# Kernel optimization log

Measured on AMD Instinct MI355X. Metric: run time of the kernel, lower is better.

## Reference

```python
import jax, jax.numpy as jnp
import numpy as np

ALPHA = 0.2          # LeakyReLU negative slope
N = 4096             # num nodes
E = 262144           # num edges (avg degree 64)
NFEAT = 512
NHID = 64
NHEAD = 8
NCLASS = 16
NEG_INF = -1e20


def setup_inputs() -> dict:
    key = jax.random.key(0)
    ks = jax.random.split(key, 8)
    features = jax.random.normal(ks[0], (N, NFEAT), dtype=jnp.float32)
    edge_list = jax.random.randint(ks[1], (2, E), 0, N, dtype=jnp.int64)
    # xavier-uniform-ish init scaled like gain=1.414
    W_heads = jax.random.normal(ks[2], (NHEAD, NFEAT, NHID), dtype=jnp.float32) * (1.414 / np.sqrt(NFEAT))
    a_heads = jax.random.normal(ks[3], (NHEAD, 2 * NHID, 1), dtype=jnp.float32) * 0.1
    b_heads = jnp.zeros((NHEAD, NHID), dtype=jnp.float32)
    W_out = jax.random.normal(ks[4], (NHEAD * NHID, NCLASS), dtype=jnp.float32) * (1.414 / np.sqrt(NHEAD * NHID))
    a_out = jax.random.normal(ks[5], (2 * NCLASS, 1), dtype=jnp.float32) * 0.1
    b_out = jnp.zeros((NCLASS,), dtype=jnp.float32)
    return {
        "features": features, "edge_list": edge_list,
        "W_heads": W_heads, "a_heads": a_heads, "b_heads": b_heads,
        "W_out": W_out, "a_out": a_out, "b_out": b_out,
    }


def _gatconv(x, src, tgt, W, a, b):
    # dropout layers are identity in eval mode
    h = x @ W                                             # [N, F_out]
    # edge scores: gather endpoints, concat, project, LeakyReLU
    a_input = jnp.concatenate([h[src], h[tgt]], axis=1)   # [E, 2*F_out]
    e = jax.nn.leaky_relu((a_input @ a)[:, 0], ALPHA)     # [E]
    n = h.shape[0]
    # dense NxN attention: -1e20 default, edge scores scattered in
    att = jnp.full((n, n), NEG_INF, dtype=h.dtype).at[src, tgt].set(e)
    att = jax.nn.softmax(att, axis=1)                     # rows w/o edges -> uniform (matches torch)
    return att @ h + b                                    # [N, F_out]


def reference(features, edge_list, W_heads, a_heads, b_heads, W_out, a_out, b_out):
    src, tgt = edge_list[0], edge_list[1]
    # multi-head GATConv, heads vmapped over stacked params -> [H, N, NHID]
    heads = jax.vmap(lambda W, a, b: _gatconv(features, src, tgt, W, a, b))(
        W_heads, a_heads, b_heads)
    # torch.cat over heads on dim=1 == transpose+reshape
    x = jnp.transpose(heads, (1, 0, 2)).reshape(N, NHEAD * NHID)
    x = jax.nn.elu(x)
    out = _gatconv(x, src, tgt, W_out, a_out, b_out)      # [N, NCLASS]
    return jax.nn.log_softmax(out, axis=1)
```

## Files before the change

kernel.cpp:

```cpp
#include <hip/hip_runtime.h>
#include <hip/hip_bf16.h>

#define NN 4096
#define NFEAT 512
#define NHID 64
#define NHEAD 8
#define NCLASS 16
#define CAP 160
#define LALPHA 0.2f

#define SZ2 (NHEAD*2*NHID)
#define SZ3 (NHEAD*NHID)
#define SZ4 (NFEAT*NCLASS)
#define SZ5 (2*NCLASS)
#define SZ6 (NCLASS)
#define NSMALL (SZ2+SZ3+SZ4+SZ5+SZ6)
#define NGB 128

typedef __attribute__((ext_vector_type(8))) short bf16x8;
typedef __attribute__((ext_vector_type(4))) float f32x4;
typedef __attribute__((ext_vector_type(8))) unsigned short u16x8;

__device__ __forceinline__ float b2f(unsigned short h) {
    return __uint_as_float(((unsigned int)h) << 16);
}
__device__ __forceinline__ unsigned short f2b(float f) {
    unsigned int u = __float_as_uint(f);
    unsigned int r = (u + 0x7fffu + ((u >> 16) & 1u)) >> 16;
    return (unsigned short)r;
}
__device__ __forceinline__ float waveMax(float v) {
#pragma unroll
    for (int m = 32; m >= 1; m >>= 1) v = fmaxf(v, __shfl_xor(v, m, 64));
    return v;
}
__device__ __forceinline__ float waveSum(float v) {
#pragma unroll
    for (int m = 32; m >= 1; m >>= 1) v += __shfl_xor(v, m, 64);
    return v;
}
__device__ __forceinline__ float lrelu(float e) {
    return e >= 0.f ? e : LALPHA * e;
}

#if defined(__has_builtin)
#if __has_builtin(__builtin_amdgcn_fence)
#define GAT_HAS_FENCE 1
#endif
#endif
#ifdef GAT_HAS_FENCE
#define REL_FENCE() __builtin_amdgcn_fence(__ATOMIC_RELEASE, "agent")
#define ACQ_FENCE() __builtin_amdgcn_fence(__ATOMIC_ACQUIRE, "agent")
#else
#define REL_FENCE() __threadfence()
#define ACQ_FENCE() __threadfence()
#endif

__device__ __forceinline__ void gbar(int* gb, int idx, int nblk) {
    __syncthreads();
    if (threadIdx.x == 0) {
        REL_FENCE();
        int* ctr  = gb + idx * 32;
        int* flag = gb + idx * 32 + 16;
        int prev = __hip_atomic_fetch_add(ctr, 1, __ATOMIC_RELAXED,
                                          __HIP_MEMORY_SCOPE_AGENT);
        if (prev == nblk - 1) {
            __hip_atomic_store(flag, 1, __ATOMIC_RELAXED,
                               __HIP_MEMORY_SCOPE_AGENT);
        } else {
            while (__hip_atomic_load(flag, __ATOMIC_RELAXED,
                                     __HIP_MEMORY_SCOPE_AGENT) == 0)
                __builtin_amdgcn_s_sleep(8);
        }
        ACQ_FENCE();
    }
    __syncthreads();
}

__global__ void __launch_bounds__(256, 4)
k01(const void* __restrict__ f, const void* __restrict__ Wh_,
    const void* __restrict__ ah_, const void* __restrict__ bh_,
    const void* __restrict__ Wo_, const void* __restrict__ ao_,
    const void* __restrict__ bo_, const int* __restrict__ e32,
    int E, int csb,
    unsigned short* __restrict__ featb, unsigned short* __restrict__ Wtb,
    float* __restrict__ smallf, unsigned int* __restrict__ bits,
    unsigned short* __restrict__ Hb,
    float* __restrict__ s1, float* __restrict__ s2,
    float* __restrict__ cm1, int* __restrict__ gb) {
    __shared__ float tile[64][33];
    __shared__ float cms[64];
    __shared__ int sbf, s64f;
    int t = threadIdx.x, bid = blockIdx.x, nblk = gridDim.x;
    if (t < 64) {
        unsigned int w = ((const unsigned int*)f)[t];
        unsigned int lo = w & 0xffffu, e = (lo >> 7) & 0xffu;
        unsigned long long bal = __ballot(lo == 0u || (e >= 100u && e <= 140u));
        if (t == 0) sbf = (__popcll(bal) >= 40);
        unsigned long long bal2 = __ballot(e32[2 * t + 1] == 0);
        if (t == 0) s64f = (__popcll(bal2) >= 48);
    }
    __syncthreads();
    bool bf = (sbf != 0);
    for (int i = bid * 256 + t; i < NN * NN / 32; i += nblk * 256)
        bits[i] = 0u;
    for (int vb = bid; vb < 128; vb += nblk) {
        int h = vb >> 4, k0 = (vb & 15) * 32;
        int nn = t & 63, kh = t >> 6;
#pragma unroll
        for (int i = 0; i < 8; ++i) {
            int kk = kh * 8 + i;
            int si = (h << 15) + (k0 + kk) * NHID + nn;
            float v = bf ? b2f(((const unsigned short*)Wh_)[si])
                         : ((const float*)Wh_)[si];
            tile[nn][kk] = v;
        }
        __syncthreads();
        int n2 = t >> 2, kk0 = (t & 3) * 8;
        u16x8 o;
#pragma unroll
        for (int i = 0; i < 8; ++i) o[i] = f2b(tile[n2][kk0 + i]);
        *(u16x8*)&Wtb[(size_t)((h << 6) + n2) * NFEAT + k0 + kk0] = o;
        __syncthreads();
    }
    {
        const int NF8 = NN * NFEAT / 8;
        const int TOT = NF8 + NSMALL;
        int start = bf ? NF8 : 0;
        for (int i = start + bid * 256 + t; i < TOT; i += nblk * 256) {
            if (i < NF8) {
                float4 lo = ((const float4*)f)[i * 2];
                float4 hi = ((const float4*)f)[i * 2 + 1];
                u16x8 o;
                o[0] = f2b(lo.x); o[1] = f2b(lo.y); o[2] = f2b(lo.z); o[3] = f2b(lo.w);
                o[4] = f2b(hi.x); o[5] = f2b(hi.y); o[6] = f2b(hi.z); o[7] = f2b(hi.w);
                *(u16x8*)&featb[i * 8] = o;
            } else {
                int r = i - NF8;
                const void* sp; int off;
                if (r < SZ2)                        { sp = ah_; off = r; }
                else if (r < SZ2 + SZ3)             { sp = bh_; off = r - SZ2; }
                else if (r < SZ2 + SZ3 + SZ4)       { sp = Wo_; off = r - SZ2 - SZ3; }
                else if (r < SZ2 + SZ3 + SZ4 + SZ5) { sp = ao_; off = r - SZ2 - SZ3 - SZ4; }
                else                                { sp = bo_; off = r - SZ2 - SZ3 - SZ4 - SZ5; }
                smallf[r] = bf ? b2f(((const unsigned short*)sp)[off])
                               : ((const float*)sp)[off];
            }
        }
    }
    gbar(gb, 0, nblk);
    const unsigned short* Ab = bf ? (const unsigned short*)f : featb;
    const float* av8 = smallf;
    for (int tl = bid; tl < 256; tl += nblk) {
        if (t < 64) cms[t] = 0.f;
        __syncthreads();
        int w = t >> 6, l = t & 63;
        int quad = l >> 4, l16 = l & 15;
        int h = tl >> 5;
        int m0 = (tl & 31) * 128 + w * 32;
        f32x4 acc[2][4] = {};
        const unsigned short* a0p = Ab + (size_t)(m0 + l16) * NFEAT + quad * 8;
        const unsigned short* a1p = a0p + 16 * NFEAT;
        const unsigned short* bp  = Wtb + ((size_t)h << 15) + (size_t)l16 * NFEAT + quad * 8;
#pragma unroll 4
        for (int k0 = 0; k0 < NFEAT; k0 += 32) {
            bf16x8 a0 = *(const bf16x8*)(a0p + k0);
            bf16x8 a1 = *(const bf16x8*)(a1p + k0);
#pragma unroll
            for (int nt = 0; nt < 4; ++nt) {
                bf16x8 b = *(const bf16x8*)(bp + (size_t)nt * 16 * NFEAT + k0);
                acc[0][nt] = __builtin_amdgcn_mfma_f32_16x16x32_bf16(a0, b, acc[0][nt], 0, 0, 0);
                acc[1][nt] = __builtin_amdgcn_mfma_f32_16x16x32_bf16(a1, b, acc[1][nt], 0, 0, 0);
            }
        }
        const float* av = av8 + h * 2 * NHID;
        float p1[2][4] = {}, p2[2][4] = {};
#pragma unroll
        for (int rh = 0; rh < 2; ++rh) {
#pragma unroll
            for (int nt = 0; nt < 4; ++nt) {
                int col = nt * 16 + l16;
                float av1 = av[col], av2 = av[NHID + col];
                float csum = 0.f;
#pragma unroll
                for (int r = 0; r < 4; ++r) {
                    float v = acc[rh][nt][r];
                    int row = m0 + rh * 16 + quad * 4 + r;
                    Hb[((size_t)row << 9) + (h << 6) + col] = f2b(v);
                    p1[rh][r] += v * av1;
                    p2[rh][r] += v * av2;
                    csum += v;
                }
                atomicAdd(&cms[col], csum);
            }
        }
#pragma unroll
        for (int m = 8; m >= 1; m >>= 1)
#pragma unroll
            for (int rh = 0; rh < 2; ++rh)
#pragma unroll
                for (int r = 0; r < 4; ++r) {
                    p1[rh][r] += __shfl_xor(p1[rh][r], m, 64);
                    p2[rh][r] += __shfl_xor(p2[rh][r], m, 64);
                }
        if (l16 == 0) {
#pragma unroll
            for (int rh = 0; rh < 2; ++rh)
#pragma unroll
                for (int r = 0; r < 4; ++r) {
                    int row = m0 + rh * 16 + quad * 4 + r;
                    s1[(h << 12) + row] = p1[rh][r];
                    s2[(h << 12) + row] = p2[rh][r];
                }
        }
        __syncthreads();
        if (t < 64) atomicAdd(&cm1[h * NHID + t], cms[t]);
        __syncthreads();
    }
    for (int vb = bid; vb < csb; vb += nblk) {
        int i = vb * 256 + t;
        if (i < E) {
            int s, tt;
            if (s64f) { s = e32[2 * i]; tt = e32[2 * (E + i)]; }
            else      { s = e32[i];     tt = e32[E + i]; }
            s &= (NN - 1); tt &= (NN - 1);
            unsigned int pos = (unsigned int)s * NN + (unsigned int)tt;
            atomicOr(&bits[pos >> 5], 1u << (pos & 31u));
        }
    }
}

__global__ void __launch_bounds__(256, 4)
k23(const unsigned int* __restrict__ bits,
    const float* __restrict__ s1, const float* __restrict__ s2,
    const unsigned short* __restrict__ Hb,
    const float* __restrict__ bh, const float* __restrict__ cm1,
    const float* __restrict__ Wo, const float* __restrict__ ao,
    const float* __restrict__ bo,
    float* __restrict__ out2, float* __restrict__ s1o,
    float* __restrict__ s2o, float* __restrict__ cm2,
    float* __restrict__ outp, int* __restrict__ gb) {
    __shared__ float sW[4][CAP * 8];
    __shared__ int   sT[4][CAP];
    __shared__ float cms[NCLASS];
    __shared__ float o2s[4][16];
    int t = threadIdx.x, bid = blockIdx.x, nblk = gridDim.x;
    if (t < NCLASS) cms[t] = 0.f;
    int wid = t >> 6, lane = t & 63;
    int n = bid * 4 + wid;
    int d;
    {
        uint2 w2 = *(const uint2*)&bits[n * 128 + lane * 2];
        int c = __popc(w2.x) + __popc(w2.y);
        int incl = c;
#pragma unroll
        for (int off = 1; off < 64; off <<= 1) {
            int u = __shfl_up(incl, off, 64);
            if (lane >= off) incl += u;
        }
        int excl = incl - c;
        int total = __shfl(incl, 63, 64);
        int tbase = lane * 64;
        unsigned int x = w2.x;
        while (x) {
            int b = __ffs(x) - 1; x &= x - 1;
            if (excl < CAP) sT[wid][excl] = tbase + b;
            ++excl;
        }
        unsigned int y = w2.y;
        while (y) {
            int b = __ffs(y) - 1; y &= y - 1;
            if (excl < CAP) sT[wid][excl] = tbase + 32 + b;
            ++excl;
        }
        d = min(total, CAP);
    }
    __syncthreads();
    int h = lane >> 3, jslot = lane & 7;
    float acc[8] = {};
    float rden = 1.f;
    if (d > 0) {
        const float* s2h = s2 + ((size_t)h << 12);
        float s1n = s1[(h << 12) + n];
        float mx = -1e30f;
        for (int jb = 0; jb < d; jb += 8) {
            int j = jb + jslot;
            int tt = (j < d) ? sT[wid][j] : 0;
            float e = (j < d) ? lrelu(s1n + s2h[tt]) : -1e30f;
            sW[wid][(j << 3) + h] = e;
            mx = fmaxf(mx, e);
        }
        mx = fmaxf(mx, __shfl_xor(mx, 1, 64));
        mx = fmaxf(mx, __shfl_xor(mx, 2, 64));
        mx = fmaxf(mx, __shfl_xor(mx, 4, 64));
        float den = 0.f;
        for (int jb = 0; jb < d; jb += 8) {
            int j = jb + jslot;
            float e = sW[wid][(j << 3) + h];
            float w = __expf(e - mx);
            sW[wid][(j << 3) + h] = w;
            den += w;
        }
        den += __shfl_xor(den, 1, 64);
        den += __shfl_xor(den, 2, 64);
        den += __shfl_xor(den, 4, 64);
        rden = 1.f / den;
        const unsigned short* Hp = Hb + lane * 8;
        int j = 0;
        for (; j + 8 <= d; j += 8) {
            int tt[8]; float ww[8];
#pragma unroll
            for (int q = 0; q < 8; ++q) {
                tt[q] = sT[wid][j + q];
                ww[q] = sW[wid][((j + q) << 3) + h];
            }
            u16x8 vv[8];
#pragma unroll
            for (int q = 0; q < 8; ++q)
                vv[q] = *(const u16x8*)(Hp + ((size_t)tt[q] << 9));
#pragma unroll
            for (int q = 0; q < 8; ++q)
#pragma unroll
                for (int i = 0; i < 8; ++i)
                    acc[i] += ww[q] * b2f(vv[q][i]);
        }
        for (; j < d; ++j) {
            int t0 = sT[wid][j];
            float w0 = sW[wid][(j << 3) + h];
            u16x8 v0 = *(const u16x8*)(Hp + ((size_t)t0 << 9));
#pragma unroll
            for (int i = 0; i < 8; ++i) acc[i] += w0 * b2f(v0[i]);
        }
    }
    float o[8];
    if (d == 0) {
#pragma unroll
        for (int i = 0; i < 8; ++i) o[i] = cm1[lane * 8 + i] * (1.0f / NN);
    } else {
#pragma unroll
        for (int i = 0; i < 8; ++i) o[i] = acc[i] * rden;
    }
#pragma unroll
    for (int i = 0; i < 8; ++i) {
        float v = o[i] + bh[lane * 8 + i];
        o[i] = v > 0.f ? v : __expf(v) - 1.f;
    }
    float* xw = sW[wid];
    *(float4*)&xw[lane * 8]     = make_float4(o[0], o[1], o[2], o[3]);
    *(float4*)&xw[lane * 8 + 4] = make_float4(o[4], o[5], o[6], o[7]);
    int c = lane & 15, sub = lane >> 4;
    const float* xp = xw + sub * 128;
    const float* wp = Wo + sub * 128 * NCLASS + c;
    float a2 = 0.f;
#pragma unroll 8
    for (int kk = 0; kk < 128; ++kk) a2 += xp[kk] * wp[kk * NCLASS];
    a2 += __shfl_xor(a2, 16, 64);
    a2 += __shfl_xor(a2, 32, 64);
    if (lane < 16) out2[n * NCLASS + c] = a2;
    float r1 = a2 * ao[c], r2 = a2 * ao[NCLASS + c];
#pragma unroll
    for (int m = 8; m >= 1; m >>= 1) {
        r1 += __shfl_xor(r1, m, 16);
        r2 += __shfl_xor(r2, m, 16);
    }
    if (lane == 0) { s1o[n] = r1; s2o[n] = r2; }
    if (lane < 16) atomicAdd(&cms[c], a2);
    __syncthreads();
    if (t < NCLASS) atomicAdd(&cm2[t], cms[t]);

    gbar(gb, 1, nblk);

    {
        float val;
        if (d == 0) {
            val = cm2[c] * (1.0f / NN);
        } else {
            float s1n = s1o[n];
            float* wvw = sW[wid];
            int t0 = (lane < d)       ? sT[wid][lane]       : 0;
            int t1 = (lane + 64 < d)  ? sT[wid][lane + 64]  : 0;
            int t2 = (lane + 128 < d) ? sT[wid][lane + 128] : 0;
            float e0 = (lane < d)       ? lrelu(s1n + s2o[t0]) : -1e30f;
            float e1 = (lane + 64 < d)  ? lrelu(s1n + s2o[t1]) : -1e30f;
            float e2 = (lane + 128 < d) ? lrelu(s1n + s2o[t2]) : -1e30f;
            float m = waveMax(fmaxf(e0, fmaxf(e1, e2)));
            float w0 = (lane < d)       ? __expf(e0 - m) : 0.f;
            float w1 = (lane + 64 < d)  ? __expf(e1 - m) : 0.f;
            float w2 = (lane + 128 < d) ? __expf(e2 - m) : 0.f;
            float den = waveSum(w0 + w1 + w2);
            wvw[lane] = w0;
            wvw[lane + 64] = w1;
            if (lane + 128 < CAP) wvw[lane + 128] = w2;
            int g2 = lane >> 2, q = lane & 3;
            float a4[4] = {};
            for (int j = g2; j < d; j += 16) {
                float w = wvw[j];
                int tt = sT[wid][j];
                float4 v = *(const float4*)(out2 + tt * NCLASS + q * 4);
                a4[0] += w * v.x; a4[1] += w * v.y;
                a4[2] += w * v.z; a4[3] += w * v.w;
            }
#pragma unroll
            for (int m2 = 4; m2 <= 32; m2 <<= 1)
#pragma unroll
                for (int i = 0; i < 4; ++i) a4[i] += __shfl_xor(a4[i], m2, 64);
            if (lane < 4)
                *(float4*)&o2s[wid][lane * 4] = make_float4(a4[0], a4[1], a4[2], a4[3]);
            val = o2s[wid][c] / den;
        }
        val += bo[c];
        float mx = val;
#pragma unroll
        for (int m = 8; m >= 1; m >>= 1) mx = fmaxf(mx, __shfl_xor(mx, m, 16));
        float se = __expf(val - mx);
#pragma unroll
        for (int m = 8; m >= 1; m >>= 1) se += __shfl_xor(se, m, 16);
        float res = val - mx - __logf(se);
        if (lane < 16) outp[n * NCLASS + lane] = res;
    }
}

__global__ void __launch_bounds__(256)
k_prep0(const void* __restrict__ f, const void* __restrict__ Wh_,
        const void* __restrict__ ah_, const void* __restrict__ bh_,
        const void* __restrict__ Wo_, const void* __restrict__ ao_,
        const void* __restrict__ bo_,
        unsigned short* __restrict__ featb,
        unsigned short* __restrict__ Wtb,
        float* __restrict__ smallf,
        unsigned int* __restrict__ bits,
        float* __restrict__ cmz) {
    int t = threadIdx.x, bid = blockIdx.x;
    for (int i = bid * 256 + t; i < NN * NN / 32; i += gridDim.x * 256)
        bits[i] = 0u;
    if (bid == 0)
        for (int i = t; i < NHEAD * NHID + NCLASS; i += 256) cmz[i] = 0.f;
    __shared__ int sbf;
    if (t < 64) {
        unsigned int w = ((const unsigned int*)f)[t];
        unsigned int lo = w & 0xffffu, e = (lo >> 7) & 0xffu;
        unsigned long long bal = __ballot(lo == 0u || (e >= 100u && e <= 140u));
        if (t == 0) sbf = (__popcll(bal) >= 40);
    }
    __syncthreads();
    bool bf = (sbf != 0);
    if (bid < 128) {
        __shared__ float tile[64][33];
        int h = bid >> 4, k0 = (bid & 15) * 32;
        int n = t & 63, kh = t >> 6;
#pragma unroll
        for (int i = 0; i < 8; ++i) {
            int kk = kh * 8 + i;
            int si = (h << 15) + (k0 + kk) * NHID + n;
            float v = bf ? b2f(((const unsigned short*)Wh_)[si])
                         : ((const float*)Wh_)[si];
            tile[n][kk] = v;
        }
        __syncthreads();
        int n2 = t >> 2, kk0 = (t & 3) * 8;
        u16x8 o;
#pragma unroll
        for (int i = 0; i < 8; ++i) o[i] = f2b(tile[n2][kk0 + i]);
        *(u16x8*)&Wtb[(size_t)((h << 6) + n2) * NFEAT + k0 + kk0] = o;
    } else {
        const int NF8 = NN * NFEAT / 8;
        const int TOT = NF8 + NSMALL;
        int stride = (gridDim.x - 128) * 256;
        int start = bf ? NF8 : 0;
        for (int i = start + (bid - 128) * 256 + t; i < TOT; i += stride) {
            if (i < NF8) {
                float4 lo = ((const float4*)f)[i * 2];
                float4 hi = ((const float4*)f)[i * 2 + 1];
                u16x8 o;
                o[0] = f2b(lo.x); o[1] = f2b(lo.y); o[2] = f2b(lo.z); o[3] = f2b(lo.w);
                o[4] = f2b(hi.x); o[5] = f2b(hi.y); o[6] = f2b(hi.z); o[7] = f2b(hi.w);
                *(u16x8*)&featb[i * 8] = o;
            } else {
                int r = i - NF8;
                const void* sp; int off;
                if (r < SZ2)                        { sp = ah_; off = r; }
                else if (r < SZ2 + SZ3)             { sp = bh_; off = r - SZ2; }
                else if (r < SZ2 + SZ3 + SZ4)       { sp = Wo_; off = r - SZ2 - SZ3; }
                else if (r < SZ2 + SZ3 + SZ4 + SZ5) { sp = ao_; off = r - SZ2 - SZ3 - SZ4; }
                else                                { sp = bo_; off = r - SZ2 - SZ3 - SZ4 - SZ5; }
                smallf[r] = bf ? b2f(((const unsigned short*)sp)[off])
                               : ((const float*)sp)[off];
            }
        }
    }
}

__global__ void __launch_bounds__(256)
k_gemm_or(const void* __restrict__ f,
          const unsigned short* __restrict__ featb,
          const unsigned short* __restrict__ Wtb,
          const float* __restrict__ ah,
          unsigned short* __restrict__ Hb,
          float* __restrict__ s1, float* __restrict__ s2,
          float* __restrict__ cm1,
          const int* __restrict__ e32, int E,
          unsigned int* __restrict__ bits) {
    int t = threadIdx.x;
    if (blockIdx.x >= 256) {
        __shared__ int s64f;
        if (t < 64) {
            unsigned long long bal = __ballot(e32[2 * t + 1] == 0);
            if (t == 0) s64f = (__popcll(bal) >= 48);
        }
        __syncthreads();
        int i = (blockIdx.x - 256) * 256 + t;
        if (i < E) {
            int s, tt;
            if (s64f) { s = e32[2 * i]; tt = e32[2 * (E + i)]; }
            else      { s = e32[i];     tt = e32[E + i]; }
            s &= (NN - 1); tt &= (NN - 1);
            unsigned int pos = (unsigned int)s * NN + (unsigned int)tt;
            atomicOr(&bits[pos >> 5], 1u << (pos & 31u));
        }
        return;
    }
    __shared__ int sbf;
    if (t < 64) {
        unsigned int w = ((const unsigned int*)f)[t];
        unsigned int lo = w & 0xffffu, e = (lo >> 7) & 0xffu;
        unsigned long long bal = __ballot(lo == 0u || (e >= 100u && e <= 140u));
        if (t == 0) sbf = (__popcll(bal) >= 40);
    }
    __shared__ float cms[64];
    if (t < 64) cms[t] = 0.f;
    __syncthreads();
    const unsigned short* Ab = sbf ? (const unsigned short*)f : featb;
    int w = t >> 6, l = t & 63;
    int quad = l >> 4, l16 = l & 15;
    int h = blockIdx.x >> 5;
    int m0 = (blockIdx.x & 31) * 128 + w * 32;
    f32x4 acc[2][4] = {};
    const unsigned short* a0p = Ab + (size_t)(m0 + l16) * NFEAT + quad * 8;
    const unsigned short* a1p = a0p + 16 * NFEAT;
    const unsigned short* bp  = Wtb + ((size_t)h << 15) + (size_t)l16 * NFEAT + quad * 8;
#pragma unroll 4
    for (int k0 = 0; k0 < NFEAT; k0 += 32) {
        bf16x8 a0 = *(const bf16x8*)(a0p + k0);
        bf16x8 a1 = *(const bf16x8*)(a1p + k0);
#pragma unroll
        for (int nt = 0; nt < 4; ++nt) {
            bf16x8 b = *(const bf16x8*)(bp + (size_t)nt * 16 * NFEAT + k0);
            acc[0][nt] = __builtin_amdgcn_mfma_f32_16x16x32_bf16(a0, b, acc[0][nt], 0, 0, 0);
            acc[1][nt] = __builtin_amdgcn_mfma_f32_16x16x32_bf16(a1, b, acc[1][nt], 0, 0, 0);
        }
    }
    const float* av = ah + h * 2 * NHID;
    float p1[2][4] = {}, p2[2][4] = {};
#pragma unroll
    for (int rh = 0; rh < 2; ++rh) {
#pragma unroll
        for (int nt = 0; nt < 4; ++nt) {
            int col = nt * 16 + l16;
            float av1 = av[col], av2 = av[NHID + col];
            float csum = 0.f;
#pragma unroll
            for (int r = 0; r < 4; ++r) {
                float v = acc[rh][nt][r];
                int row = m0 + rh * 16 + quad * 4 + r;
                Hb[((size_t)row << 9) + (h << 6) + col] = f2b(v);
                p1[rh][r] += v * av1;
                p2[rh][r] += v * av2;
                csum += v;
            }
            atomicAdd(&cms[col], csum);
        }
    }
#pragma unroll
    for (int m = 8; m >= 1; m >>= 1)
#pragma unroll
        for (int rh = 0; rh < 2; ++rh)
#pragma unroll
            for (int r = 0; r < 4; ++r) {
                p1[rh][r] += __shfl_xor(p1[rh][r], m, 64);
                p2[rh][r] += __shfl_xor(p2[rh][r], m, 64);
            }
    if (l16 == 0) {
#pragma unroll
        for (int rh = 0; rh < 2; ++rh)
#pragma unroll
            for (int r = 0; r < 4; ++r) {
                int row = m0 + rh * 16 + quad * 4 + r;
                s1[(h << 12) + row] = p1[rh][r];
                s2[(h << 12) + row] = p2[rh][r];
            }
    }
    __syncthreads();
    if (t < 64) atomicAdd(&cm1[h * NHID + t], cms[t]);
}

__global__ void __launch_bounds__(256)
k_eattn1(const unsigned int* __restrict__ bits,
         int* __restrict__ deg, int* __restrict__ csr,
         const float* __restrict__ s1, const float* __restrict__ s2,
         const unsigned short* __restrict__ Hb,
         const float* __restrict__ bh, const float* __restrict__ cm1,
         const float* __restrict__ Wo, const float* __restrict__ ao,
         float* __restrict__ out2, float* __restrict__ s1o,
         float* __restrict__ s2o, float* __restrict__ cm2) {
    __shared__ float sW[4][CAP * 8];
    __shared__ int   sT[4][CAP];
    __shared__ float cms[NCLASS];
    int t = threadIdx.x;
    if (t < NCLASS) cms[t] = 0.f;
    int wid = t >> 6, lane = t & 63;
    int n = blockIdx.x * 4 + wid;
    int d;
    {
        uint2 w2 = *(const uint2*)&bits[n * 128 + lane * 2];
        int c = __popc(w2.x) + __popc(w2.y);
        int incl = c;
#pragma unroll
        for (int off = 1; off < 64; off <<= 1) {
            int u = __shfl_up(incl, off, 64);
            if (lane >= off) incl += u;
        }
        int excl = incl - c;
        int total = __shfl(incl, 63, 64);
        if (lane == 0) deg[n] = total;
        int tbase = lane * 64;
        unsigned int x = w2.x;
        while (x) {
            int b = __ffs(x) - 1; x &= x - 1;
            if (excl < CAP) sT[wid][excl] = tbase + b;
            ++excl;
        }
        unsigned int y = w2.y;
        while (y) {
            int b = __ffs(y) - 1; y &= y - 1;
            if (excl < CAP) sT[wid][excl] = tbase + 32 + b;
            ++excl;
        }
        d = min(total, CAP);
    }
    __syncthreads();
    for (int k = lane; k < d; k += 64) csr[(size_t)n * CAP + k] = sT[wid][k];
    int h = lane >> 3, jslot = lane & 7;
    float acc[8] = {};
    float rden = 1.f;
    if (d > 0) {
        const float* s2h = s2 + ((size_t)h << 12);
        float s1n = s1[(h << 12) + n];
        float mx = -1e30f;
        for (int jb = 0; jb < d; jb += 8) {
            int j = jb + jslot;
            int tt = (j < d) ? sT[wid][j] : 0;
            float e = (j < d) ? lrelu(s1n + s2h[tt]) : -1e30f;
            sW[wid][(j << 3) + h] = e;
            mx = fmaxf(mx, e);
        }
        mx = fmaxf(mx, __shfl_xor(mx, 1, 64));
        mx = fmaxf(mx, __shfl_xor(mx, 2, 64));
        mx = fmaxf(mx, __shfl_xor(mx, 4, 64));
        float den = 0.f;
        for (int jb = 0; jb < d; jb += 8) {
            int j = jb + jslot;
            float e = sW[wid][(j << 3) + h];
            float w = __expf(e - mx);
            sW[wid][(j << 3) + h] = w;
            den += w;
        }
        den += __shfl_xor(den, 1, 64);
        den += __shfl_xor(den, 2, 64);
        den += __shfl_xor(den, 4, 64);
        rden = 1.f / den;
        const unsigned short* Hp = Hb + lane * 8;
        int j = 0;
        for (; j + 8 <= d; j += 8) {
            int tt[8]; float ww[8];
#pragma unroll
            for (int q = 0; q < 8; ++q) {
                tt[q] = sT[wid][j + q];
                ww[q] = sW[wid][((j + q) << 3) + h];
            }
            u16x8 vv[8];
#pragma unroll
            for (int q = 0; q < 8; ++q)
                vv[q] = *(const u16x8*)(Hp + ((size_t)tt[q] << 9));
#pragma unroll
            for (int q = 0; q < 8; ++q)
#pragma unroll
                for (int i = 0; i < 8; ++i)
                    acc[i] += ww[q] * b2f(vv[q][i]);
        }
        for (; j < d; ++j) {
            int t0 = sT[wid][j];
            float w0 = sW[wid][(j << 3) + h];
            u16x8 v0 = *(const u16x8*)(Hp + ((size_t)t0 << 9));
#pragma unroll
            for (int i = 0; i < 8; ++i) acc[i] += w0 * b2f(v0[i]);
        }
    }
    float o[8];
    if (d == 0) {
#pragma unroll
        for (int i = 0; i < 8; ++i) o[i] = cm1[lane * 8 + i] * (1.0f / NN);
    } else {
#pragma unroll
        for (int i = 0; i < 8; ++i) o[i] = acc[i] * rden;
    }
#pragma unroll
    for (int i = 0; i < 8; ++i) {
        float v = o[i] + bh[lane * 8 + i];
        o[i] = v > 0.f ? v : __expf(v) - 1.f;
    }
    float* xw = sW[wid];
    *(float4*)&xw[lane * 8]     = make_float4(o[0], o[1], o[2], o[3]);
    *(float4*)&xw[lane * 8 + 4] = make_float4(o[4], o[5], o[6], o[7]);
    int c = lane & 15, sub = lane >> 4;
    const float* xp = xw + sub * 128;
    const float* wp = Wo + sub * 128 * NCLASS + c;
    float a2 = 0.f;
#pragma unroll 8
    for (int kk = 0; kk < 128; ++kk) a2 += xp[kk] * wp[kk * NCLASS];
    a2 += __shfl_xor(a2, 16, 64);
    a2 += __shfl_xor(a2, 32, 64);
    if (lane < 16) out2[n * NCLASS + c] = a2;
    float r1 = a2 * ao[c], r2 = a2 * ao[NCLASS + c];
#pragma unroll
    for (int m = 8; m >= 1; m >>= 1) {
        r1 += __shfl_xor(r1, m, 16);
        r2 += __shfl_xor(r2, m, 16);
    }
    if (lane == 0) { s1o[n] = r1; s2o[n] = r2; }
    if (lane < 16) atomicAdd(&cms[c], a2);
    __syncthreads();
    if (t < NCLASS) atomicAdd(&cm2[t], cms[t]);
}

__global__ void __launch_bounds__(256)
k_attn2(const int* __restrict__ deg, const int* __restrict__ csr,
        const float* __restrict__ s1o, const float* __restrict__ s2o,
        const float* __restrict__ out2, const float* __restrict__ bo,
        const float* __restrict__ cm2, float* __restrict__ outp) {
    __shared__ float wv[4][CAP];
    __shared__ float o2s[4][16];
    int wid = threadIdx.x >> 6, lane = threadIdx.x & 63;
    int n = blockIdx.x * 4 + wid;
    int c = lane & 15;
    int d = min(deg[n], CAP);
    float val;
    if (d == 0) {
        val = cm2[c] * (1.0f / NN);
    } else {
        float s1n = s1o[n];
        const int* rowp = csr + (size_t)n * CAP;
        int t0 = (lane < d)       ? rowp[lane]       : 0;
        int t1 = (lane + 64 < d)  ? rowp[lane + 64]  : 0;
        int t2 = (lane + 128 < d) ? rowp[lane + 128] : 0;
        float e0 = (lane < d)       ? lrelu(s1n + s2o[t0]) : -1e30f;
        float e1 = (lane + 64 < d)  ? lrelu(s1n + s2o[t1]) : -1e30f;
        float e2 = (lane + 128 < d) ? lrelu(s1n + s2o[t2]) : -1e30f;
        float m = waveMax(fmaxf(e0, fmaxf(e1, e2)));
        float w0 = (lane < d)       ? __expf(e0 - m) : 0.f;
        float w1 = (lane + 64 < d)  ? __expf(e1 - m) : 0.f;
        float w2 = (lane + 128 < d) ? __expf(e2 - m) : 0.f;
        float den = waveSum(w0 + w1 + w2);
        wv[wid][lane] = w0;
        if (lane + 64 < CAP)  wv[wid][lane + 64]  = w1;
        if (lane + 128 < CAP) wv[wid][lane + 128] = w2;
        int g2 = lane >> 2, q = lane & 3;
        float a4[4] = {};
        for (int j = g2; j < d; j += 16) {
            float w = wv[wid][j];
            int tt = rowp[j];
            float4 v = *(const float4*)(out2 + tt * NCLASS + q * 4);
            a4[0] += w * v.x; a4[1] += w * v.y;
            a4[2] += w * v.z; a4[3] += w * v.w;
        }
#pragma unroll
        for (int m2 = 4; m2 <= 32; m2 <<= 1)
#pragma unroll
            for (int i = 0; i < 4; ++i) a4[i] += __shfl_xor(a4[i], m2, 64);
        if (lane < 4)
            *(float4*)&o2s[wid][lane * 4] = make_float4(a4[0], a4[1], a4[2], a4[3]);
        val = o2s[wid][c] / den;
    }
    val += bo[c];
    float mx = val;
#pragma unroll
    for (int m = 8; m >= 1; m >>= 1) mx = fmaxf(mx, __shfl_xor(mx, m, 16));
    float se = __expf(val - mx);
#pragma unroll
    for (int m = 8; m >= 1; m >>= 1) se += __shfl_xor(se, m, 16);
    float res = val - mx - __logf(se);
    if (lane < 16) outp[n * NCLASS + lane] = res;
}

extern "C" void kernel_launch(void* const* d_in, const int* in_sizes, int n_in,
                              void* d_out, int out_size, void* d_ws, size_t ws_size,
                              hipStream_t stream) {
    const void* features = d_in[0];
    const int*  edges    = (const int*)d_in[1];
    const void* W_heads  = d_in[2];
    const void* a_heads  = d_in[3];
    const void* b_heads  = d_in[4];
    const void* W_out    = d_in[5];
    const void* a_out    = d_in[6];
    const void* b_out    = d_in[7];
    int E = in_sizes[1] / 2;
    int csb = (E + 255) / 256;

    int*   gb   = (int*)d_ws;
    float* cm1  = (float*)(gb + NGB);
    float* cm2  = cm1 + NHEAD * NHID;
    unsigned int* bits = (unsigned int*)(cm2 + NCLASS);
    int*   deg  = (int*)(bits + (NN * NN / 32));
    int*   csr  = deg + NN;
    float* s1   = (float*)(csr + NN * CAP);
    float* s2   = s1 + NHEAD * NN;
    float* out2 = s2 + NHEAD * NN;
    float* s1o  = out2 + NN * NCLASS;
    float* s2o  = s1o + NN;
    float* smallf = s2o + NN;
    unsigned short* Hb    = (unsigned short*)(smallf + NSMALL);
    unsigned short* featb = Hb + (size_t)NN * NHEAD * NHID;
    unsigned short* Wtb   = featb + (size_t)NN * NFEAT;
    float* outp = (float*)d_out;
    const float* bhf = smallf + SZ2;
    const float* Wof = smallf + SZ2 + SZ3;
    const float* aof = Wof + SZ4;
    const float* bof = aof + SZ5;

    static int cap01 = -2, cap23 = -2;
    if (cap01 == -2) {
        int b01 = 0, b23 = 0, ncu = 0, dev = 0;
        (void)hipGetDevice(&dev);
        if (hipDeviceGetAttribute(&ncu, hipDeviceAttributeMultiprocessorCount, dev)
                != hipSuccess) ncu = 0;
        if (hipOccupancyMaxActiveBlocksPerMultiprocessor(
                &b01, reinterpret_cast<const void*>(&k01), 256, 0) != hipSuccess) b01 = 0;
        if (hipOccupancyMaxActiveBlocksPerMultiprocessor(
                &b23, reinterpret_cast<const void*>(&k23), 256, 0) != hipSuccess) b23 = 0;
        cap01 = (b01 > 0 && ncu > 0) ? b01 * ncu : 0;
        cap23 = (b23 > 0 && ncu > 0) ? b23 * ncu : 0;
    }
    int nblk01 = cap01 > 1024 ? 1024 : cap01;

    if (nblk01 >= 128 && cap23 >= NN / 4) {
        hipMemsetAsync(d_ws, 0, (size_t)(NGB + NHEAD * NHID + NCLASS) * 4, stream);
        hipLaunchKernelGGL(k01, dim3(nblk01), dim3(256), 0, stream,
                           features, W_heads, a_heads, b_heads, W_out, a_out, b_out,
                           edges, E, csb, featb, Wtb, smallf, bits, Hb, s1, s2, cm1, gb);
        hipLaunchKernelGGL(k23, dim3(NN / 4), dim3(256), 0, stream,
                           bits, s1, s2, Hb, bhf, cm1, Wof, aof, bof,
                           out2, s1o, s2o, cm2, outp, gb);
    } else {
        hipLaunchKernelGGL(k_prep0, dim3(2048), dim3(256), 0, stream,
                           features, W_heads, a_heads, b_heads, W_out, a_out, b_out,
                           featb, Wtb, smallf, bits, cm1);
        hipLaunchKernelGGL(k_gemm_or, dim3(256 + csb), dim3(256), 0, stream,
                           features, featb, Wtb, smallf, Hb, s1, s2, cm1, edges, E, bits);
        hipLaunchKernelGGL(k_eattn1, dim3(NN / 4), dim3(256), 0, stream,
                           bits, deg, csr, s1, s2, Hb, bhf, cm1, Wof, aof,
                           out2, s1o, s2o, cm2);
        hipLaunchKernelGGL(k_attn2, dim3(NN / 4), dim3(256), 0, stream,
                           deg, csr, s1o, s2o, out2, bof, cm2, outp);
    }
}
```

Measured before the change: 142.2 us.

## Split each node's neighbor aggregation across two waves in k23

k23 now assigns two wavefronts per node instead of one: each half processes half the neighbor list for scores, softmax max/denominator and the bf16 feature gather, with partial results combined through shared memory. The grid doubles to NN/2 blocks, and launch bounds ask for 8 blocks per CU so the grid-barrier residency check still passes. The aim is more memory-level parallelism on the gather-heavy first-layer aggregation. The cost is extra __syncthreads and shared-memory merge steps, and the second wave idles during the output projection and second-layer attention.

```diff
diff --git a/kernel.cpp b/kernel.cpp
--- a/kernel.cpp
+++ b/kernel.cpp
@@ -230,7 +230,7 @@
     }
 }
 
-__global__ void __launch_bounds__(256, 4)
+__global__ void __launch_bounds__(256, 8)
 k23(const unsigned int* __restrict__ bits,
     const float* __restrict__ s1, const float* __restrict__ s2,
     const unsigned short* __restrict__ Hb,
@@ -240,16 +240,19 @@
     float* __restrict__ out2, float* __restrict__ s1o,
     float* __restrict__ s2o, float* __restrict__ cm2,
     float* __restrict__ outp, int* __restrict__ gb) {
-    __shared__ float sW[4][CAP * 8];
-    __shared__ int   sT[4][CAP];
+    __shared__ float sW[2][CAP * 8];
+    __shared__ int   sT[2][CAP];
+    __shared__ int   sDeg[2];
+    __shared__ float sMx[2][2][8];
+    __shared__ float sDen[2][2][8];
     __shared__ float cms[NCLASS];
-    __shared__ float o2s[4][16];
+    __shared__ float o2s[2][16];
     int t = threadIdx.x, bid = blockIdx.x, nblk = gridDim.x;
     if (t < NCLASS) cms[t] = 0.f;
     int wid = t >> 6, lane = t & 63;
-    int n = bid * 4 + wid;
-    int d;
-    {
+    int nl = wid >> 1, jhalf = wid & 1;
+    int n = bid * 2 + nl;
+    if (jhalf == 0) {
         uint2 w2 = *(const uint2*)&bits[n * 128 + lane * 2];
         int c = __popc(w2.x) + __popc(w2.y);
         int incl = c;
@@ -260,22 +263,26 @@
         }
         int excl = incl - c;
         int total = __shfl(incl, 63, 64);
+        if (lane == 0) sDeg[nl] = total;
         int tbase = lane * 64;
         unsigned int x = w2.x;
         while (x) {
             int b = __ffs(x) - 1; x &= x - 1;
-            if (excl < CAP) sT[wid][excl] = tbase + b;
+            if (excl < CAP) sT[nl][excl] = tbase + b;
             ++excl;
         }
         unsigned int y = w2.y;
         while (y) {
             int b = __ffs(y) - 1; y &= y - 1;
-            if (excl < CAP) sT[wid][excl] = tbase + 32 + b;
+            if (excl < CAP) sT[nl][excl] = tbase + 32 + b;
             ++excl;
         }
-        d = min(total, CAP);
-    }
-    __syncthreads();
+    }
+    __syncthreads();
+    int d = min(sDeg[nl], CAP);
+    int dh = (d + 1) >> 1;
+    int j0 = jhalf ? dh : 0;
+    int j1 = jhalf ? d : dh;
     int h = lane >> 3, jslot = lane & 7;
     float acc[8] = {};
     float rden = 1.f;
@@ -283,36 +290,49 @@
         const float* s2h = s2 + ((size_t)h << 12);
         float s1n = s1[(h << 12) + n];
         float mx = -1e30f;
-        for (int jb = 0; jb < d; jb += 8) {
+        for (int jb = j0; jb < j1; jb += 8) {
             int j = jb + jslot;
-            int tt = (j < d) ? sT[wid][j] : 0;
-            float e = (j < d) ? lrelu(s1n + s2h[tt]) : -1e30f;
-            sW[wid][(j << 3) + h] = e;
-            mx = fmaxf(mx, e);
+            if (j < j1) {
+                int tt = sT[nl][j];
+                float e = lrelu(s1n + s2h[tt]);
+                sW[nl][(j << 3) + h] = e;
+                mx = fmaxf(mx, e);
+            }
         }
         mx = fmaxf(mx, __shfl_xor(mx, 1, 64));
         mx = fmaxf(mx, __shfl_xor(mx, 2, 64));
         mx = fmaxf(mx, __shfl_xor(mx, 4, 64));
+        if (jslot == 0) sMx[nl][jhalf][h] = mx;
+    }
+    __syncthreads();
+    if (d > 0) {
+        float mx = fmaxf(sMx[nl][0][h], sMx[nl][1][h]);
         float den = 0.f;
-        for (int jb = 0; jb < d; jb += 8) {
+        for (int jb = j0; jb < j1; jb += 8) {
             int j = jb + jslot;
-            float e = sW[wid][(j << 3) + h];
-            float w = __expf(e - mx);
-            sW[wid][(j << 3) + h] = w;
-            den += w;
+            if (j < j1) {
+                float e = sW[nl][(j << 3) + h];
+                float w = __expf(e - mx);
+                sW[nl][(j << 3) + h] = w;
+                den += w;
+            }
         }
         den += __shfl_xor(den, 1, 64);
         den += __shfl_xor(den, 2, 64);
         den += __shfl_xor(den, 4, 64);
-        rden = 1.f / den;
+        if (jslot == 0) sDen[nl][jhalf][h] = den;
+    }
+    __syncthreads();
+    if (d > 0) {
+        rden = 1.f / (sDen[nl][0][h] + sDen[nl][1][h]);
         const unsigned short* Hp = Hb + lane * 8;
-        int j = 0;
-        for (; j + 8 <= d; j += 8) {
+        int j = j0;
+        for (; j + 8 <= j1; j += 8) {
             int tt[8]; float ww[8];
 #pragma unroll
             for (int q = 0; q < 8; ++q) {
-                tt[q] = sT[wid][j + q];
-                ww[q] = sW[wid][((j + q) << 3) + h];
+                tt[q] = sT[nl][j + q];
+                ww[q] = sW[nl][((j + q) << 3) + h];
             }
             u16x8 vv[8];
 #pragma unroll
@@ -324,62 +344,71 @@
                 for (int i = 0; i < 8; ++i)
                     acc[i] += ww[q] * b2f(vv[q][i]);
         }
-        for (; j < d; ++j) {
-            int t0 = sT[wid][j];
-            float w0 = sW[wid][(j << 3) + h];
+        for (; j < j1; ++j) {
+            int t0 = sT[nl][j];
+            float w0 = sW[nl][(j << 3) + h];
             u16x8 v0 = *(const u16x8*)(Hp + ((size_t)t0 << 9));
 #pragma unroll
             for (int i = 0; i < 8; ++i) acc[i] += w0 * b2f(v0[i]);
         }
     }
-    float o[8];
-    if (d == 0) {
-#pragma unroll
-        for (int i = 0; i < 8; ++i) o[i] = cm1[lane * 8 + i] * (1.0f / NN);
-    } else {
-#pragma unroll
-        for (int i = 0; i < 8; ++i) o[i] = acc[i] * rden;
-    }
-#pragma unroll
-    for (int i = 0; i < 8; ++i) {
-        float v = o[i] + bh[lane * 8 + i];
-        o[i] = v > 0.f ? v : __expf(v) - 1.f;
-    }
-    float* xw = sW[wid];
-    *(float4*)&xw[lane * 8]     = make_float4(o[0], o[1], o[2], o[3]);
-    *(float4*)&xw[lane * 8 + 4] = make_float4(o[4], o[5], o[6], o[7]);
-    int c = lane & 15, sub = lane >> 4;
-    const float* xp = xw + sub * 128;
-    const float* wp = Wo + sub * 128 * NCLASS + c;
-    float a2 = 0.f;
+    __syncthreads();
+    float* comb = sW[nl];
+    if (jhalf == 1) {
+        *(float4*)&comb[lane * 8]     = make_float4(acc[0], acc[1], acc[2], acc[3]);
+        *(float4*)&comb[lane * 8 + 4] = make_float4(acc[4], acc[5], acc[6], acc[7]);
+    }
+    __syncthreads();
+    if (jhalf == 0) {
+        float o[8];
+        if (d == 0) {
+#pragma unroll
+            for (int i = 0; i < 8; ++i) o[i] = cm1[lane * 8 + i] * (1.0f / NN);
+        } else {
+#pragma unroll
+            for (int i = 0; i < 8; ++i) o[i] = (acc[i] + comb[lane * 8 + i]) * rden;
+        }
+#pragma unroll
+        for (int i = 0; i < 8; ++i) {
+            float v = o[i] + bh[lane * 8 + i];
+            o[i] = v > 0.f ? v : __expf(v) - 1.f;
+        }
+        *(float4*)&comb[lane * 8]     = make_float4(o[0], o[1], o[2], o[3]);
+        *(float4*)&comb[lane * 8 + 4] = make_float4(o[4], o[5], o[6], o[7]);
+        int c = lane & 15, sub = lane >> 4;
+        const float* xp = comb + sub * 128;
+        const float* wp = Wo + sub * 128 * NCLASS + c;
+        float a2 = 0.f;
 #pragma unroll 8
-    for (int kk = 0; kk < 128; ++kk) a2 += xp[kk] * wp[kk * NCLASS];
-    a2 += __shfl_xor(a2, 16, 64);
-    a2 += __shfl_xor(a2, 32, 64);
-    if (lane < 16) out2[n * NCLASS + c] = a2;
-    float r1 = a2 * ao[c], r2 = a2 * ao[NCLASS + c];
-#pragma unroll
-    for (int m = 8; m >= 1; m >>= 1) {
-        r1 += __shfl_xor(r1, m, 16);
-        r2 += __shfl_xor(r2, m, 16);
-    }
-    if (lane == 0) { s1o[n] = r1; s2o[n] = r2; }
-    if (lane < 16) atomicAdd(&cms[c], a2);
+        for (int kk = 0; kk < 128; ++kk) a2 += xp[kk] * wp[kk * NCLASS];
+        a2 += __shfl_xor(a2, 16, 64);
+        a2 += __shfl_xor(a2, 32, 64);
+        if (lane < 16) out2[n * NCLASS + c] = a2;
+        float r1 = a2 * ao[c], r2 = a2 * ao[NCLASS + c];
+#pragma unroll
+        for (int m = 8; m >= 1; m >>= 1) {
+            r1 += __shfl_xor(r1, m, 16);
+            r2 += __shfl_xor(r2, m, 16);
+        }
+        if (lane == 0) { s1o[n] = r1; s2o[n] = r2; }
+        if (lane < 16) atomicAdd(&cms[c], a2);
+    }
     __syncthreads();
     if (t < NCLASS) atomicAdd(&cm2[t], cms[t]);
 
     gbar(gb, 1, nblk);
 
-    {
+    if (jhalf == 0) {
+        int c = lane & 15;
         float val;
         if (d == 0) {
             val = cm2[c] * (1.0f / NN);
         } else {
             float s1n = s1o[n];
-            float* wvw = sW[wid];
-            int t0 = (lane < d)       ? sT[wid][lane]       : 0;
-            int t1 = (lane + 64 < d)  ? sT[wid][lane + 64]  : 0;
-            int t2 = (lane + 128 < d) ? sT[wid][lane + 128] : 0;
+            float* wvw = sW[nl];
+            int t0 = (lane < d)       ? sT[nl][lane]       : 0;
+            int t1 = (lane + 64 < d)  ? sT[nl][lane + 64]  : 0;
+            int t2 = (lane + 128 < d) ? sT[nl][lane + 128] : 0;
             float e0 = (lane < d)       ? lrelu(s1n + s2o[t0]) : -1e30f;
             float e1 = (lane + 64 < d)  ? lrelu(s1n + s2o[t1]) : -1e30f;
             float e2 = (lane + 128 < d) ? lrelu(s1n + s2o[t2]) : -1e30f;
@@ -395,7 +424,7 @@
             float a4[4] = {};
             for (int j = g2; j < d; j += 16) {
                 float w = wvw[j];
-                int tt = sT[wid][j];
+                int tt = sT[nl][j];
                 float4 v = *(const float4*)(out2 + tt * NCLASS + q * 4);
                 a4[0] += w * v.x; a4[1] += w * v.y;
                 a4[2] += w * v.z; a4[3] += w * v.w;
@@ -405,8 +434,8 @@
 #pragma unroll
                 for (int i = 0; i < 4; ++i) a4[i] += __shfl_xor(a4[i], m2, 64);
             if (lane < 4)
-                *(float4*)&o2s[wid][lane * 4] = make_float4(a4[0], a4[1], a4[2], a4[3]);
-            val = o2s[wid][c] / den;
+                *(float4*)&o2s[nl][lane * 4] = make_float4(a4[0], a4[1], a4[2], a4[3]);
+            val = o2s[nl][c] / den;
         }
         val += bo[c];
         float mx = val;
@@ -841,12 +870,12 @@
     }
     int nblk01 = cap01 > 1024 ? 1024 : cap01;
 
-    if (nblk01 >= 128 && cap23 >= NN / 4) {
+    if (nblk01 >= 128 && cap23 >= NN / 2) {
         hipMemsetAsync(d_ws, 0, (size_t)(NGB + NHEAD * NHID + NCLASS) * 4, stream);
         hipLaunchKernelGGL(k01, dim3(nblk01), dim3(256), 0, stream,
                            features, W_heads, a_heads, b_heads, W_out, a_out, b_out,
                            edges, E, csb, featb, Wtb, smallf, bits, Hb, s1, s2, cm1, gb);
-        hipLaunchKernelGGL(k23, dim3(NN / 4), dim3(256), 0, stream,
+        hipLaunchKernelGGL(k23, dim3(NN / 2), dim3(256), 0, stream,
                            bits, s1, s2, Hb, bhf, cm1, Wof, aof, bof,
                            out2, s1o, s2o, cm2, outp, gb);
     } else {
```

Result: no change. 141.8 us (-0.3%).
